# Kernel optimization log

Hardware: AMD Instinct MI355X
Metric: run time of the kernel (lower is better)

The kernel has to match this reference:

```python
import jax, jax.numpy as jnp
import numpy as np

WH, WW = 16, 16
NUM_HEADS = 16
DIM = 1024
BATCH = 64
SEQ = WH * WW + 1  # 257, includes cls token
NUM_REL = (2 * WH - 1) * (2 * WW - 1) + 3  # 964


def _make_rel_pos_index(wh, ww):
    # BEiT relative position index construction (intended semantics of the torch code)
    coords = np.stack(np.meshgrid(np.arange(wh), np.arange(ww), indexing='ij'))  # [2, wh, ww]
    flat = coords.reshape(2, -1)  # [2, wh*ww]
    rel = flat[:, :, None] - flat[:, None, :]  # [2, N-1, N-1]
    rel = rel.transpose(1, 2, 0).astype(np.int64)
    rel[:, :, 0] += wh - 1
    rel[:, :, 1] += ww - 1
    rel[:, :, 0] *= 2 * ww - 1
    num_rel = (2 * wh - 1) * (2 * ww - 1) + 3
    idx = np.zeros((wh * ww + 1, wh * ww + 1), dtype=np.int32)
    idx[1:, 1:] = rel.sum(-1)
    idx[0, :] = num_rel - 3  # cls-to-token
    idx[:, 0] = num_rel - 2  # token-to-cls
    idx[0, 0] = num_rel - 1  # cls-to-cls
    return idx


def setup_inputs() -> dict:
    key = jax.random.key(0)
    ks = jax.random.split(key, 7)
    return {
        'x': jax.random.normal(ks[0], (BATCH, SEQ, DIM), dtype=jnp.float32),
        'qkv_weight': jax.random.normal(ks[1], (3 * DIM, DIM), dtype=jnp.float32) * 0.02,
        'query_bias': jax.random.normal(ks[2], (DIM,), dtype=jnp.float32) * 0.02,
        'value_bias': jax.random.normal(ks[3], (DIM,), dtype=jnp.float32) * 0.02,
        'rel_pos_bias_table': jax.random.normal(ks[4], (NUM_REL, NUM_HEADS), dtype=jnp.float32) * 0.02,
        'proj_weight': jax.random.normal(ks[5], (DIM, DIM), dtype=jnp.float32) * 0.02,
        'proj_bias': jax.random.normal(ks[6], (DIM,), dtype=jnp.float32) * 0.02,
        'rel_pos_index': jnp.asarray(_make_rel_pos_index(WH, WW)),
    }


def reference(x, qkv_weight, query_bias, value_bias, rel_pos_bias_table,
              proj_weight, proj_bias, rel_pos_index):
    B, N, C = x.shape
    H = rel_pos_bias_table.shape[-1]
    D = qkv_weight.shape[0] // 3 // H
    scale = D ** -0.5
    # qkv bias: (q_bias, zeros, v_bias) as in the torch module
    qkv_bias = jnp.concatenate([query_bias, jnp.zeros_like(value_bias), value_bias])
    qkv = x @ qkv_weight.T + qkv_bias  # [B, N, 3*H*D]
    qkv = qkv.reshape(B, N, 3, H, D).transpose(2, 0, 3, 1, 4)  # [3, B, H, N, D]
    q, k, v = qkv[0] * scale, qkv[1], qkv[2]
    attn = jnp.einsum('bhqd,bhkd->bhqk', q, k)  # [B, H, N, N]
    bias = rel_pos_bias_table[rel_pos_index]  # [N, N, H]
    attn = attn + bias.transpose(2, 0, 1)[None]  # add per-head bias
    attn = jax.nn.softmax(attn, axis=-1)
    out = jnp.einsum('bhqk,bhkd->bhqd', attn, v)  # [B, H, N, D]
    out = out.transpose(0, 2, 1, 3).reshape(B, N, H * D)
    return out @ proj_weight.T + proj_bias
```

## Files before the change

### kernel.cpp

```cpp
#include <hip/hip_runtime.h>


typedef unsigned short u16;
typedef __attribute__((ext_vector_type(8))) short bf16x8;
typedef __attribute__((ext_vector_type(4))) float f32x4;

#define MFMA16(a, b, c) __builtin_amdgcn_mfma_f32_16x16x32_bf16(a, b, c, 0, 0, 0)
#define GLDS16(g, l)                                                           \
  __builtin_amdgcn_global_load_lds(                                            \
      (const __attribute__((address_space(1))) void*)(g),                      \
      (__attribute__((address_space(3))) void*)(l), 16, 0, 0)

#define QOFF 0
#define KOFF 16842752
#define VTOFF 33685504
#define VTP 264

__device__ __forceinline__ u16 f2bf(float f) {
  unsigned u = __builtin_bit_cast(unsigned, f);
  u += 0x7FFFu + ((u >> 16) & 1u);
  return (u16)(u >> 16);
}
__device__ __forceinline__ unsigned pack2(float a, float b) {
  return (unsigned)f2bf(a) | ((unsigned)f2bf(b) << 16);
}

__global__ __launch_bounds__(256) void cvt_bf16(const float* __restrict__ in,
                                                u16* __restrict__ out, int n4) {
  int i = blockIdx.x * 256 + threadIdx.x;
  if (i < n4) {
    float4 v = ((const float4*)in)[i];
    uint2 o;
    o.x = pack2(v.x, v.y);
    o.y = pack2(v.z, v.w);
    ((uint2*)out)[i] = o;
  }
}

__global__ __launch_bounds__(256) void bias_pre(const float* __restrict__ tab,
                                                const int* __restrict__ idx,
                                                float* __restrict__ out) {
  int t = blockIdx.x * 256 + threadIdx.x;
  if (t < 66049) {
    int id = idx[t];
    const float* row = tab + (size_t)id * 16;
#pragma unroll
    for (int h = 0; h < 16; h++)
      out[(size_t)h * 66049 + t] = row[h] * 1.4426950408889634f;
  }
}


#define GEMM_PROLOG(M_, K_)                                                    \
  __shared__ __align__(16) u16 SMEM[16384];                                    \
  u16* const As = SMEM;                                                        \
  u16* const Bs = SMEM + 8192;                                                 \
  const int M = (M_), K = (K_);                                                \
  const int tid = threadIdx.x;                                                 \
  const int lane = tid & 63, wave = tid >> 6;                                  \
  const int quad = lane >> 4, l15 = lane & 15;                                 \
  const int wr = (wave >> 1) * 64, wc = (wave & 1) * 64;                       \
  const int m0 = blockIdx.y * 128, n0 = blockIdx.x * 128;                      \
  const int sgk = ((tid & 7) ^ ((tid >> 3) & 7)) * 8;    \
  const int fo0 = (quad ^ (l15 & 7)) * 8;            \
  const int fo1 = ((4 + quad) ^ (l15 & 7)) * 8;      \
  const u16* pa0 = A + (size_t)(m0 + (tid >> 3)) * K + sgk;                    \
  const u16* pb0 = B + (size_t)(n0 + (tid >> 3)) * K + sgk;                    \
  f32x4 acc[4][4];                                                             \
  _Pragma("unroll") for (int i = 0; i < 4; i++)                                \
  _Pragma("unroll") for (int j = 0; j < 4; j++)                                \
      acc[i][j] = (f32x4){0.f, 0.f, 0.f, 0.f};                                 \
  for (int k0 = 0; k0 < K; k0 += 64) {                                         \
    __syncthreads();                                                           \
    _Pragma("unroll") for (int b = 0; b < 4; b++) {                            \
      GLDS16(pa0 + k0 + (size_t)b * 32 * K, As + b * 2048 + tid * 8);          \
      GLDS16(pb0 + k0 + (size_t)b * 32 * K, Bs + b * 2048 + tid * 8);          \
    }                                                                          \
    __syncthreads();                                                           \
    _Pragma("unroll") for (int kk = 0; kk < 2; kk++) {                         \
      const int fo = kk ? fo1 : fo0;                                           \
      bf16x8 bfr[4];                                                           \
      _Pragma("unroll") for (int t = 0; t < 4; t++)                            \
          bfr[t] = *(const bf16x8*)(Bs + (wc + t * 16 + l15) * 64 + fo);       \
      _Pragma("unroll") for (int i = 0; i < 4; i++) {                          \
        bf16x8 afr = *(const bf16x8*)(As + (wr + i * 16 + l15) * 64 + fo);     \
        _Pragma("unroll") for (int j = 0; j < 4; j++)                          \
            acc[i][j] = MFMA16(afr, bfr[j], acc[i][j]);                        \
      }                                                                        \
    }                                                                          \
  }

__global__ __launch_bounds__(256, 4) void gemm_qkv(
    const u16* __restrict__ A, const u16* __restrict__ B,
    const float* __restrict__ qbias, const float* __restrict__ vbias,
    u16* __restrict__ C) {
  GEMM_PROLOG(16448, 1024)
  if (n0 >= 2048) {
    u16* const T = SMEM;
    for (int p = 0; p < 2; p++) {
      __syncthreads();
      if ((wave & 1) == p) {
#pragma unroll
        for (int j = 0; j < 4; j++) {
          int cl = j * 16 + l15;
          int rem = (n0 + wc + j * 16 + l15) & 1023;
          float vb_ = vbias[rem];
          int swz = (cl & 15) << 3;
#pragma unroll
          for (int i = 0; i < 4; i++) {
            int rlb = wr + i * 16 + quad * 4;
#pragma unroll
            for (int rr = 0; rr < 2; rr++) {
              unsigned pk = pack2(acc[i][j][rr * 2] + vb_,
                                  acc[i][j][rr * 2 + 1] + vb_);
              *(unsigned*)(T + cl * 128 + ((rlb + rr * 2) ^ swz)) = pk;
            }
          }
        }
      }
      __syncthreads();
#pragma unroll
      for (int cc = 0; cc < 16; cc++) {
        int cl = cc * 4 + wave;
        int rem = (n0 + p * 64 + cl) & 1023;
        int h = rem >> 6, d = rem & 63;
        size_t cb = (size_t)VTOFF + ((size_t)h * 64 + d) * VTP;
        int swz = (cl & 15) << 3;
#pragma unroll
        for (int half = 0; half < 2; half++) {
          int rl = half * 64 + lane;
          u16 val = T[cl * 128 + (rl ^ swz)];
          int m = m0 + rl;
          if (m < M) {
            unsigned bb2 = (unsigned)m / 257u;
            unsigned nn2 = (unsigned)m - bb2 * 257u;
            C[cb + (size_t)bb2 * (16 * 64 * VTP) + nn2] = val;
          }
        }
      }
    }
  } else {
#pragma unroll
    for (int i = 0; i < 4; i++) {
#pragma unroll
      for (int r = 0; r < 4; r++) {
        int row = m0 + wr + i * 16 + quad * 4 + r;
        if (row < M) {
          unsigned bb = (unsigned)row / 257u;
          unsigned nn = (unsigned)row - bb * 257u;
#pragma unroll
          for (int j = 0; j < 4; j++) {
            int c = n0 + wc + j * 16 + l15;
            int which = c >> 10, rem = c & 1023;
            float bias = (which == 0) ? qbias[rem] : 0.f;
            float v = acc[i][j][r] + bias;
            if (which == 0) v *= 0.18033688011112042f;
            int h = rem >> 6, d = rem & 63;
            size_t dst = (size_t)which * 16842752 +
                         (size_t)(bb * 16 + h) * 16448 + (size_t)nn * 64 + d;
            C[dst] = f2bf(v);
          }
        }
      }
    }
  }
}

__global__ __launch_bounds__(256, 4) void gemm_proj(
    const u16* __restrict__ A, const u16* __restrict__ B,
    const float* __restrict__ pbias, float* __restrict__ C) {
  GEMM_PROLOG(16448, 1024)
#pragma unroll
  for (int i = 0; i < 4; i++) {
#pragma unroll
    for (int r = 0; r < 4; r++) {
      int row = m0 + wr + i * 16 + quad * 4 + r;
      if (row < M) {
#pragma unroll
        for (int j = 0; j < 4; j++) {
          int c = n0 + wc + j * 16 + l15;
          C[(size_t)row * 1024 + c] = acc[i][j][r] + pbias[c];
        }
      }
    }
  }
}

__global__ __launch_bounds__(256, 3) void attn_fused(
    const u16* __restrict__ qkv, const float* __restrict__ biasT,
    u16* __restrict__ out) {
  __shared__ __align__(16) u16 KVs[96 * 72];
  __shared__ __align__(16) u16 Ps[4 * 16 * 104];
  const int bx = blockIdx.x;
  const int qt = bx % 5, bh = bx / 5;
  const int b = bh >> 4, h = bh & 15;
  const int tid = threadIdx.x, lane = tid & 63, wave = tid >> 6;
  const int quad = lane >> 4, l15 = lane & 15;
  const u16* qg = qkv + QOFF + (size_t)bh * 16448;
  const u16* kg = qkv + KOFF + (size_t)bh * 16448;
  const u16* vtg = qkv + VTOFF + (size_t)bh * (64 * VTP);

  int qra = qt * 64 + wave * 16 + l15;
  if (qra > 256) qra = 256;
  const bf16x8 aq0 = *(const bf16x8*)(qg + (size_t)qra * 64 + quad * 8);
  const bf16x8 aq1 = *(const bf16x8*)(qg + (size_t)qra * 64 + 32 + quad * 8);

  const int qbase = qt * 64 + wave * 16 + quad * 4;
  const float* bb = biasT + (size_t)h * 66049;
  f32x4 s[18];
#pragma unroll
  for (int r = 0; r < 4; r++) {
    int qr = qbase + r;
    if (qr > 256) qr = 256;
    const float* brow = bb + (size_t)qr * 257;
#pragma unroll
    for (int t = 0; t < 18; t++) {
      int kc = t * 16 + l15;
      s[t][r] = (kc < 257) ? brow[kc] : -3e38f;
    }
  }

  const bf16x8 zv = {0, 0, 0, 0, 0, 0, 0, 0};
  for (int ck = 0; ck < 3; ck++) {
    __syncthreads();
#pragma unroll
    for (int it = 0; it < 3; it++) {
      int g = it * 256 + tid;
      int row = g >> 3, col = (g & 7) * 8;
      int gr = ck * 96 + row;
      bf16x8 kv = (gr < 257) ? *(const bf16x8*)(kg + (size_t)gr * 64 + col) : zv;
      *(bf16x8*)(KVs + row * 72 + col) = kv;
    }
    __syncthreads();
#pragma unroll
    for (int nt = 0; nt < 6; nt++) {
      bf16x8 b0 = *(const bf16x8*)(KVs + (nt * 16 + l15) * 72 + quad * 8);
      bf16x8 b1 = *(const bf16x8*)(KVs + (nt * 16 + l15) * 72 + 32 + quad * 8);
      int t = ck * 6 + nt;
      s[t] = MFMA16(aq0, b0, s[t]);
      s[t] = MFMA16(aq1, b1, s[t]);
    }
  }

  float inv[4];
#pragma unroll
  for (int r = 0; r < 4; r++) {
    float m = -3e38f;
#pragma unroll
    for (int t = 0; t < 18; t++) m = fmaxf(m, s[t][r]);
    m = fmaxf(m, __shfl_xor(m, 1));
    m = fmaxf(m, __shfl_xor(m, 2));
    m = fmaxf(m, __shfl_xor(m, 4));
    m = fmaxf(m, __shfl_xor(m, 8));
    float sum = 0.f;
#pragma unroll
    for (int t = 0; t < 18; t++) {
      float p = __builtin_amdgcn_exp2f(s[t][r] - m);
      s[t][r] = p;
      sum += p;
    }
    sum += __shfl_xor(sum, 1);
    sum += __shfl_xor(sum, 2);
    sum += __shfl_xor(sum, 4);
    sum += __shfl_xor(sum, 8);
    inv[r] = 1.f / sum;
  }

  u16* Pw = Ps + wave * (16 * 104);
  f32x4 o[4];
#pragma unroll
  for (int nt = 0; nt < 4; nt++) o[nt] = (f32x4){0.f, 0.f, 0.f, 0.f};
  for (int ck = 0; ck < 3; ck++) {
    __syncthreads();
#pragma unroll
    for (int it = 0; it < 3; it++) {
      int g = it * 256 + tid;
      int row = g / 12, c = (g % 12) * 8;
      bf16x8 v = *(const bf16x8*)(vtg + (size_t)row * VTP + ck * 96 + c);
      *(bf16x8*)(KVs + row * 104 + c) = v;
    }
#pragma unroll
    for (int nt = 0; nt < 6; nt++) {
      int t = ck * 6 + nt;
#pragma unroll
      for (int r = 0; r < 4; r++)
        Pw[(quad * 4 + r) * 104 + nt * 16 + l15] = f2bf(s[t][r]);
    }
    __syncthreads();
#pragma unroll
    for (int ks = 0; ks < 3; ks++) {
      bf16x8 ap = *(const bf16x8*)(Pw + l15 * 104 + ks * 32 + quad * 8);
#pragma unroll
      for (int nt = 0; nt < 4; nt++) {
        bf16x8 bv =
            *(const bf16x8*)(KVs + (nt * 16 + l15) * 104 + ks * 32 + quad * 8);
        o[nt] = MFMA16(ap, bv, o[nt]);
      }
    }
  }

#pragma unroll
  for (int nt = 0; nt < 4; nt++) {
    int d = nt * 16 + l15;
#pragma unroll
    for (int r = 0; r < 4; r++) {
      int qr = qbase + r;
      if (qr < 257)
        out[((size_t)b * 257 + qr) * 1024 + h * 64 + d] =
            f2bf(o[nt][r] * inv[r]);
    }
  }
}

extern "C" void kernel_launch(void* const* d_in, const int* in_sizes, int n_in,
                              void* d_out, int out_size, void* d_ws,
                              size_t ws_size, hipStream_t stream) {
  const float* x = (const float*)d_in[0];
  const float* qkvw = (const float*)d_in[1];
  const float* qb = (const float*)d_in[2];
  const float* vb = (const float*)d_in[3];
  const float* tab = (const float*)d_in[4];
  const float* pw = (const float*)d_in[5];
  const float* pb = (const float*)d_in[6];
  const int* rpi = (const int*)d_in[7];

  char* ws = (char*)d_ws;
  u16* qkvbuf = (u16*)ws;
  u16* xbuf = (u16*)(ws + 101974016);
  float* biasb = (float*)(ws + 135659520);
  u16* qkvwb = (u16*)(ws + 139886656);
  u16* projwb = (u16*)(ws + 146178112);

  cvt_bf16<<<16448, 256, 0, stream>>>(x, xbuf, 4210688);
  cvt_bf16<<<3072, 256, 0, stream>>>(qkvw, qkvwb, 786432);
  cvt_bf16<<<1024, 256, 0, stream>>>(pw, projwb, 262144);
  bias_pre<<<259, 256, 0, stream>>>(tab, rpi, biasb);
  gemm_qkv<<<dim3(24, 129), 256, 0, stream>>>(xbuf, qkvwb, qb, vb, qkvbuf);
  attn_fused<<<5120, 256, 0, stream>>>(qkvbuf, biasb, xbuf);
  gemm_proj<<<dim3(8, 129), 256, 0, stream>>>(xbuf, projwb, pb, (float*)d_out);
}
```

Measured before the change: 423.8 us.

## Store relative position bias as padded bf16 and remap attention block order

The precomputed bias table becomes bf16 in a padded, interleaved 288-column layout, so each lane loads one 32-bit word that holds two key columns, and padding entries hold a large negative value. This halves bias bytes and removes the per-element bounds checks. Attention blocks are remapped so that 8 consecutive blocks cover different (batch, head) pairs for the same query tile, and in the last query tile only wave 0 does work, since the other waves there hold only padding rows. Bias precision drops to bf16, which adds some numerical error to the logits.

```diff
diff --git a/kernel.cpp b/kernel.cpp
--- a/kernel.cpp
+++ b/kernel.cpp
@@ -39,14 +39,23 @@
 
 __global__ __launch_bounds__(256) void bias_pre(const float* __restrict__ tab,
                                                 const int* __restrict__ idx,
-                                                float* __restrict__ out) {
+                                                u16* __restrict__ out) {
   int t = blockIdx.x * 256 + threadIdx.x;
   if (t < 66049) {
+    int i = t / 257, j = t - i * 257;
+    int off = i * 288 + ((j >> 5) << 5) + ((j & 15) << 1) + ((j >> 4) & 1);
     int id = idx[t];
     const float* row = tab + (size_t)id * 16;
 #pragma unroll
     for (int h = 0; h < 16; h++)
-      out[(size_t)h * 66049 + t] = row[h] * 1.4426950408889634f;
+      out[(size_t)h * 74016 + off] = f2bf(row[h] * 1.4426950408889634f);
+  } else if (t < 66049 + 257 * 31) {
+    int u = t - 66049;
+    int i = u / 31, j = 257 + (u - i * 31);
+    int off = i * 288 + ((j >> 5) << 5) + ((j & 15) << 1) + ((j >> 4) & 1);
+#pragma unroll
+    for (int h = 0; h < 16; h++)
+      out[(size_t)h * 74016 + off] = 0xFF7Fu;
   }
 }
 
@@ -187,15 +196,18 @@
 }
 
 __global__ __launch_bounds__(256, 3) void attn_fused(
-    const u16* __restrict__ qkv, const float* __restrict__ biasT,
+    const u16* __restrict__ qkv, const u16* __restrict__ biasT,
     u16* __restrict__ out) {
   __shared__ __align__(16) u16 KVs[96 * 72];
   __shared__ __align__(16) u16 Ps[4 * 16 * 104];
   const int bx = blockIdx.x;
-  const int qt = bx % 5, bh = bx / 5;
+  const int xj = bx & 7, xi = bx >> 3;
+  const int qt = xi % 5;
+  const int bh = (xi / 5) * 8 + xj;
   const int b = bh >> 4, h = bh & 15;
   const int tid = threadIdx.x, lane = tid & 63, wave = tid >> 6;
   const int quad = lane >> 4, l15 = lane & 15;
+  const bool act = (qt < 4) || (wave == 0);
   const u16* qg = qkv + QOFF + (size_t)bh * 16448;
   const u16* kg = qkv + KOFF + (size_t)bh * 16448;
   const u16* vtg = qkv + VTOFF + (size_t)bh * (64 * VTP);
@@ -206,17 +218,20 @@
   const bf16x8 aq1 = *(const bf16x8*)(qg + (size_t)qra * 64 + 32 + quad * 8);
 
   const int qbase = qt * 64 + wave * 16 + quad * 4;
-  const float* bb = biasT + (size_t)h * 66049;
   f32x4 s[18];
-#pragma unroll
-  for (int r = 0; r < 4; r++) {
-    int qr = qbase + r;
-    if (qr > 256) qr = 256;
-    const float* brow = bb + (size_t)qr * 257;
-#pragma unroll
-    for (int t = 0; t < 18; t++) {
-      int kc = t * 16 + l15;
-      s[t][r] = (kc < 257) ? brow[kc] : -3e38f;
+  if (act) {
+    const u16* bb = biasT + (size_t)h * 74016;
+#pragma unroll
+    for (int r = 0; r < 4; r++) {
+      int qr = qbase + r;
+      if (qr > 256) qr = 256;
+      const unsigned* brow = (const unsigned*)(bb + (size_t)qr * 288);
+#pragma unroll
+      for (int p = 0; p < 9; p++) {
+        unsigned u = brow[p * 16 + l15];
+        s[2 * p][r] = __builtin_bit_cast(float, u << 16);
+        s[2 * p + 1][r] = __builtin_bit_cast(float, u & 0xFFFF0000u);
+      }
     }
   }
 
@@ -232,38 +247,42 @@
       *(bf16x8*)(KVs + row * 72 + col) = kv;
     }
     __syncthreads();
-#pragma unroll
-    for (int nt = 0; nt < 6; nt++) {
-      bf16x8 b0 = *(const bf16x8*)(KVs + (nt * 16 + l15) * 72 + quad * 8);
-      bf16x8 b1 = *(const bf16x8*)(KVs + (nt * 16 + l15) * 72 + 32 + quad * 8);
-      int t = ck * 6 + nt;
-      s[t] = MFMA16(aq0, b0, s[t]);
-      s[t] = MFMA16(aq1, b1, s[t]);
+    if (act) {
+#pragma unroll
+      for (int nt = 0; nt < 6; nt++) {
+        bf16x8 b0 = *(const bf16x8*)(KVs + (nt * 16 + l15) * 72 + quad * 8);
+        bf16x8 b1 = *(const bf16x8*)(KVs + (nt * 16 + l15) * 72 + 32 + quad * 8);
+        int t = ck * 6 + nt;
+        s[t] = MFMA16(aq0, b0, s[t]);
+        s[t] = MFMA16(aq1, b1, s[t]);
+      }
     }
   }
 
   float inv[4];
-#pragma unroll
-  for (int r = 0; r < 4; r++) {
-    float m = -3e38f;
-#pragma unroll
-    for (int t = 0; t < 18; t++) m = fmaxf(m, s[t][r]);
-    m = fmaxf(m, __shfl_xor(m, 1));
-    m = fmaxf(m, __shfl_xor(m, 2));
-    m = fmaxf(m, __shfl_xor(m, 4));
-    m = fmaxf(m, __shfl_xor(m, 8));
-    float sum = 0.f;
-#pragma unroll
-    for (int t = 0; t < 18; t++) {
-      float p = __builtin_amdgcn_exp2f(s[t][r] - m);
-      s[t][r] = p;
-      sum += p;
-    }
-    sum += __shfl_xor(sum, 1);
-    sum += __shfl_xor(sum, 2);
-    sum += __shfl_xor(sum, 4);
-    sum += __shfl_xor(sum, 8);
-    inv[r] = 1.f / sum;
+  if (act) {
+#pragma unroll
+    for (int r = 0; r < 4; r++) {
+      float m = -3e38f;
+#pragma unroll
+      for (int t = 0; t < 18; t++) m = fmaxf(m, s[t][r]);
+      m = fmaxf(m, __shfl_xor(m, 1));
+      m = fmaxf(m, __shfl_xor(m, 2));
+      m = fmaxf(m, __shfl_xor(m, 4));
+      m = fmaxf(m, __shfl_xor(m, 8));
+      float sum = 0.f;
+#pragma unroll
+      for (int t = 0; t < 18; t++) {
+        float p = __builtin_amdgcn_exp2f(s[t][r] - m);
+        s[t][r] = p;
+        sum += p;
+      }
+      sum += __shfl_xor(sum, 1);
+      sum += __shfl_xor(sum, 2);
+      sum += __shfl_xor(sum, 4);
+      sum += __shfl_xor(sum, 8);
+      inv[r] = 1.f / sum;
+    }
   }
 
   u16* Pw = Ps + wave * (16 * 104);
@@ -279,35 +298,41 @@
       bf16x8 v = *(const bf16x8*)(vtg + (size_t)row * VTP + ck * 96 + c);
       *(bf16x8*)(KVs + row * 104 + c) = v;
     }
-#pragma unroll
-    for (int nt = 0; nt < 6; nt++) {
-      int t = ck * 6 + nt;
-#pragma unroll
-      for (int r = 0; r < 4; r++)
-        Pw[(quad * 4 + r) * 104 + nt * 16 + l15] = f2bf(s[t][r]);
+    if (act) {
+#pragma unroll
+      for (int nt = 0; nt < 6; nt++) {
+        int t = ck * 6 + nt;
+#pragma unroll
+        for (int r = 0; r < 4; r++)
+          Pw[(quad * 4 + r) * 104 + nt * 16 + l15] = f2bf(s[t][r]);
+      }
     }
     __syncthreads();
-#pragma unroll
-    for (int ks = 0; ks < 3; ks++) {
-      bf16x8 ap = *(const bf16x8*)(Pw + l15 * 104 + ks * 32 + quad * 8);
-#pragma unroll
-      for (int nt = 0; nt < 4; nt++) {
-        bf16x8 bv =
-            *(const bf16x8*)(KVs + (nt * 16 + l15) * 104 + ks * 32 + quad * 8);
-        o[nt] = MFMA16(ap, bv, o[nt]);
-      }
-    }
-  }
-
-#pragma unroll
-  for (int nt = 0; nt < 4; nt++) {
-    int d = nt * 16 + l15;
-#pragma unroll
-    for (int r = 0; r < 4; r++) {
-      int qr = qbase + r;
-      if (qr < 257)
-        out[((size_t)b * 257 + qr) * 1024 + h * 64 + d] =
-            f2bf(o[nt][r] * inv[r]);
+    if (act) {
+#pragma unroll
+      for (int ks = 0; ks < 3; ks++) {
+        bf16x8 ap = *(const bf16x8*)(Pw + l15 * 104 + ks * 32 + quad * 8);
+#pragma unroll
+        for (int nt = 0; nt < 4; nt++) {
+          bf16x8 bv =
+              *(const bf16x8*)(KVs + (nt * 16 + l15) * 104 + ks * 32 + quad * 8);
+          o[nt] = MFMA16(ap, bv, o[nt]);
+        }
+      }
+    }
+  }
+
+  if (act) {
+#pragma unroll
+    for (int nt = 0; nt < 4; nt++) {
+      int d = nt * 16 + l15;
+#pragma unroll
+      for (int r = 0; r < 4; r++) {
+        int qr = qbase + r;
+        if (qr < 257)
+          out[((size_t)b * 257 + qr) * 1024 + h * 64 + d] =
+              f2bf(o[nt][r] * inv[r]);
+      }
     }
   }
 }
@@ -327,14 +352,14 @@
   char* ws = (char*)d_ws;
   u16* qkvbuf = (u16*)ws;
   u16* xbuf = (u16*)(ws + 101974016);
-  float* biasb = (float*)(ws + 135659520);
+  u16* biasb = (u16*)(ws + 135659520);
   u16* qkvwb = (u16*)(ws + 139886656);
   u16* projwb = (u16*)(ws + 146178112);
 
   cvt_bf16<<<16448, 256, 0, stream>>>(x, xbuf, 4210688);
   cvt_bf16<<<3072, 256, 0, stream>>>(qkvw, qkvwb, 786432);
   cvt_bf16<<<1024, 256, 0, stream>>>(pw, projwb, 262144);
-  bias_pre<<<259, 256, 0, stream>>>(tab, rpi, biasb);
+  bias_pre<<<290, 256, 0, stream>>>(tab, rpi, biasb);
   gemm_qkv<<<dim3(24, 129), 256, 0, stream>>>(xbuf, qkvwb, qb, vb, qkvbuf);
   attn_fused<<<5120, 256, 0, stream>>>(qkvbuf, biasb, xbuf);
   gemm_proj<<<dim3(8, 129), 256, 0, stream>>>(xbuf, projwb, pb, (float*)d_out);
```

Result: no change. 418.7 us (-1.2%).
